# Optimization experiments

Hardware: AMD Instinct MI355X
Metric: run time of the kernel (lower is better)

## Reference

```python
import jax, jax.numpy as jnp
import numpy as np

R = 32
EPS = 0.0
BN_EPS = 1e-5


def _voxelize(features, idx):
    # features: [C, N], idx: [N] int32 flat voxel index in [0, R^3)
    V = R * R * R
    pts = features.T  # [N, C]
    sums = jax.ops.segment_sum(pts, idx, num_segments=V)          # [V, C]
    cnts = jax.ops.segment_sum(jnp.ones_like(idx, jnp.float32), idx, num_segments=V)  # [V]
    avg = sums / jnp.maximum(cnts, 1.0)[:, None]
    mx = jax.ops.segment_max(pts, idx, num_segments=V)            # [V, C], -inf for empty
    mx = jnp.where(cnts[:, None] > 0, mx, 0.0)
    return avg, mx, cnts


def reference(features, coords, conv_w, conv_b, bn_gamma, bn_beta, bn_mean, bn_var):
    B, C, N = features.shape
    # --- coordinate normalization (coords detached in original) ---
    nc = coords - jnp.mean(coords, axis=2, keepdims=True)          # [B,3,N]
    norms = jnp.linalg.norm(nc, axis=1, keepdims=True)             # [B,1,N]
    denom = jnp.max(norms, axis=2, keepdims=True) * 2.0 + EPS      # [B,1,1]
    nc = nc / denom + 0.5
    nc = jnp.clip(nc * R, 0.0, R - 1)                              # [B,3,N]
    vox = jnp.round(nc).astype(jnp.int32)                          # [B,3,N]
    idx = vox[:, 0] * (R * R) + vox[:, 1] * R + vox[:, 2]          # [B,N]
    # --- dual scatter reduction (avg + max) per batch ---
    avg, mx, _ = jax.vmap(_voxelize)(features, idx)                # [B, V, C] each
    fea = jnp.concatenate([mx, avg], axis=-1)                      # [B, V, 2C]
    # --- 1x1 Conv3d == channel matmul ---
    y = jnp.einsum('bvc,oc->bvo', fea, conv_w) + conv_b            # [B, V, C]
    # --- BatchNorm3d (eval mode) ---
    y = (y - bn_mean) * (bn_gamma / jnp.sqrt(bn_var + BN_EPS)) + bn_beta
    # --- Swish ---
    y = y * jax.nn.sigmoid(y)
    out = jnp.transpose(y, (0, 2, 1)).reshape(B, C, R, R, R)
    return out, nc


def setup_inputs() -> dict:
    key = jax.random.key(0)
    ks = jax.random.split(key, 8)
    B, C, N = 8, 240, 16384
    return {
        'features': jax.random.normal(ks[0], (B, C, N), jnp.float32),
        'coords': jax.random.normal(ks[1], (B, 3, N), jnp.float32),
        'conv_w': jax.random.normal(ks[2], (C, 2 * C), jnp.float32) * 0.05,
        'conv_b': jax.random.normal(ks[3], (C,), jnp.float32) * 0.05,
        'bn_gamma': jnp.ones((C,), jnp.float32),
        'bn_beta': jnp.zeros((C,), jnp.float32),
        'bn_mean': jnp.zeros((C,), jnp.float32),
        'bn_var': jax.random.uniform(ks[4], (C,), jnp.float32, 0.5, 1.5),
    }
```

## Files before the change

kernel.cpp:

```cpp
#include <hip/hip_runtime.h>
#include <math.h>

#define RR 32
#define V 32768
#define C 240
#define N 16384
#define B 8
#define K2C 480
#define GZ 16
#define NGRP 2048
#define FPAD 488
#define EBUF 512

typedef __attribute__((ext_vector_type(8))) short bf16x8;
typedef __attribute__((ext_vector_type(4))) float f32x4;

__device__ __forceinline__ unsigned short f2bf(float x) {
    unsigned u = __float_as_uint(x);
    u += 0x7fffu + ((u >> 16) & 1u);
    return (unsigned short)(u >> 16);
}

__global__ __launch_bounds__(256) void prep_kernel(const float* __restrict__ feat,
                                                   unsigned short* __restrict__ featT,
                                                   const float* __restrict__ coords,
                                                   float* __restrict__ stats,
                                                   int* __restrict__ hist,
                                                   int* __restrict__ wlcnt,
                                                   const float* __restrict__ w,
                                                   unsigned short* __restrict__ w_bf) {
    __shared__ float t[C][33];
    int blk = blockIdx.x;
    int tid = threadIdx.x;
    if (blk < 4096) {
        int bx = blk & 511, b = blk >> 9;
        int n0 = bx * 32;
        int l = tid;
        const float* fb = feat + (size_t)b * C * N;
        unsigned short* fTb = featT + (size_t)b * N * C;
        int nl = l & 31, cs = l >> 5;
#pragma unroll
        for (int p = 0; p < 30; ++p) {
            int c = p * 8 + cs;
            t[c][nl] = fb[(size_t)c * N + n0 + nl];
        }
        __syncthreads();
        int ci = l & 127;
        int nh = l >> 7;
#pragma unroll
        for (int p = 0; p < 16; ++p) {
            int n = 2 * p + nh;
            if (ci < 120) {
                unsigned lo = f2bf(t[2 * ci][n]);
                unsigned hi = f2bf(t[2 * ci + 1][n]);
                *(unsigned*)&fTb[(size_t)(n0 + n) * C + 2 * ci] = lo | (hi << 16);
            }
        }
        return;
    }
    if (blk < 4352) {
        int tt = (blk - 4096) * 256 + tid;
        int4 z4 = {0, 0, 0, 0};
        ((int4*)hist)[tt] = z4;
        if (tt < 57600) {
            unsigned lo = f2bf(w[2 * tt]);
            unsigned hi = f2bf(w[2 * tt + 1]);
            ((unsigned*)w_bf)[tt] = lo | (hi << 16);
        }
        if (tt < 2 * B) wlcnt[tt] = 0;
        return;
    }
    int b = blk - 4352;
    const float* cb = coords + (size_t)b * 3 * N;
    __shared__ float red[256];
    float m[3];
    for (int d = 0; d < 3; ++d) {
        float s = 0.f;
        for (int n = tid; n < N; n += 256) s += cb[d * N + n];
        red[tid] = s; __syncthreads();
        for (int w2 = 128; w2 > 0; w2 >>= 1) { if (tid < w2) red[tid] += red[tid + w2]; __syncthreads(); }
        m[d] = red[0] / (float)N;
        __syncthreads();
    }
    float mx = 0.f;
    for (int n = tid; n < N; n += 256) {
        float dx = cb[0 * N + n] - m[0];
        float dy = cb[1 * N + n] - m[1];
        float dz = cb[2 * N + n] - m[2];
        mx = fmaxf(mx, dx * dx + dy * dy + dz * dz);
    }
    red[tid] = mx; __syncthreads();
    for (int w2 = 128; w2 > 0; w2 >>= 1) { if (tid < w2) red[tid] = fmaxf(red[tid], red[tid + w2]); __syncthreads(); }
    if (tid == 0) {
        stats[b * 4 + 0] = m[0];
        stats[b * 4 + 1] = m[1];
        stats[b * 4 + 2] = m[2];
        stats[b * 4 + 3] = 2.f * sqrtf(red[0]);
    }
}

__global__ __launch_bounds__(256) void nc_idx_kernel(const float* __restrict__ coords,
                                                     const float* __restrict__ stats,
                                                     float* __restrict__ nc_out,
                                                     int* __restrict__ idxbuf,
                                                     int* __restrict__ hist) {
    int t = blockIdx.x * 256 + threadIdx.x;
    int b = t >> 14;
    int n = t & (N - 1);
    float denom = stats[b * 4 + 3];
    int v[3];
#pragma unroll
    for (int d = 0; d < 3; ++d) {
        float x = coords[((size_t)b * 3 + d) * N + n];
        float t0 = (x - stats[b * 4 + d]) / denom + 0.5f;
        t0 = t0 * (float)RR;
        t0 = fminf(fmaxf(t0, 0.f), (float)(RR - 1));
        nc_out[((size_t)b * 3 + d) * N + n] = t0;
        v[d] = (int)rintf(t0);
    }
    int iv = v[0] * (RR * RR) + v[1] * RR + v[2];
    idxbuf[t] = iv;
    atomicAdd(hist + b * V + iv, 1);
}

__global__ __launch_bounds__(1024) void prefix_kernel(const int* __restrict__ hist,
                                                      int* __restrict__ starts,
                                                      int* __restrict__ cursor,
                                                      int* __restrict__ wl,
                                                      int* __restrict__ wlcnt) {
    __shared__ int part[1024];
    int b = blockIdx.x, t = threadIdx.x;
    int base = b * V + t * 32;
    const int4* hp = (const int4*)(hist + base);
    int4 h[8];
#pragma unroll
    for (int j = 0; j < 8; ++j) h[j] = hp[j];
    int pcA = h[0].x + h[0].y + h[0].z + h[0].w + h[1].x + h[1].y + h[1].z + h[1].w
            + h[2].x + h[2].y + h[2].z + h[2].w + h[3].x + h[3].y + h[3].z + h[3].w;
    int pcB = h[4].x + h[4].y + h[4].z + h[4].w + h[5].x + h[5].y + h[5].z + h[5].w
            + h[6].x + h[6].y + h[6].z + h[6].w + h[7].x + h[7].y + h[7].z + h[7].w;
    int s = pcA + pcB;
    if (pcA > 0) { int p = atomicAdd(wlcnt + b, 1); wl[b * NGRP + p] = 2 * t; }
    if (pcB > 0) { int p = atomicAdd(wlcnt + b, 1); wl[b * NGRP + p] = 2 * t + 1; }
    if (pcA == 0 && pcB == 0) { int q = atomicAdd(wlcnt + B + b, 1); wl[b * NGRP + NGRP - 1 - q] = (2 * t) | 0x10000; }
    else if (pcA == 0)        { int q = atomicAdd(wlcnt + B + b, 1); wl[b * NGRP + NGRP - 1 - q] = 2 * t; }
    else if (pcB == 0)        { int q = atomicAdd(wlcnt + B + b, 1); wl[b * NGRP + NGRP - 1 - q] = 2 * t + 1; }
    part[t] = s; __syncthreads();
    for (int off = 1; off < 1024; off <<= 1) {
        int x = (t >= off) ? part[t - off] : 0;
        __syncthreads();
        part[t] += x;
        __syncthreads();
    }
    int run = part[t] - s;
    int4* sp = (int4*)(starts + base);
    int4* cp = (int4*)(cursor + base);
#pragma unroll
    for (int j = 0; j < 8; ++j) {
        int4 o;
        o.x = run; run += h[j].x;
        o.y = run; run += h[j].y;
        o.z = run; run += h[j].z;
        o.w = run; run += h[j].w;
        sp[j] = o; cp[j] = o;
    }
}

__global__ __launch_bounds__(256) void plist_kernel(const int* __restrict__ idxbuf,
                                                    int* __restrict__ cursor,
                                                    int* __restrict__ ptlist) {
    int t = blockIdx.x * 256 + threadIdx.x;
    int b = t >> 14;
    int n = t & (N - 1);
    int iv = idxbuf[t];
    int pos = atomicAdd(cursor + b * V + iv, 1);
    ptlist[(b << 14) + pos] = (n << 5) | (iv & 31);
}

#define PREFETCH(U, Z0, Z1, basei)                                          \
    {                                                                       \
        Z0 = 0u; Z1 = 0u;                                                   \
        _Pragma("unroll")                                                   \
        for (int j = 0; j < 16; ++j) {                                      \
            int idx = basei + j; idx = (idx < mm) ? idx : mm - 1;           \
            int e = ebuf[idx];                                              \
            U[j] = fT[(size_t)(e >> 5) * C + c];                            \
            unsigned zz = (unsigned)(e & 15);                               \
            if (j < 8) Z0 |= zz << (4 * j); else Z1 |= zz << (4 * (j - 8)); \
        }                                                                   \
    }

#define PROCESS(U, Z0, Z1, basei)                                           \
    {                                                                       \
        _Pragma("unroll")                                                   \
        for (int j = 0; j < 16; ++j) {                                      \
            if (basei + j < mm) {                                           \
                int zj = (int)(((j < 8 ? Z0 : Z1) >> (4 * (j & 7))) & 15u); \
                if (zj != curz) {                                           \
                    if (curz >= 0) {                                        \
                        fea_s[rb + curz][c] = f2bf(mx0);                    \
                        fea_s[rb + curz][C + c] = f2bf(s0 * rcp_s[rb + curz]); \
                    }                                                       \
                    curz = zj; s0 = 0.f; mx0 = -INFINITY;                   \
                }                                                           \
                float f = __uint_as_float(((unsigned)U[j]) << 16);          \
                s0 += f; mx0 = fmaxf(mx0, f);                               \
            }                                                               \
        }                                                                   \
    }

__global__ __launch_bounds__(256, 4) void column_kernel(
    const unsigned short* __restrict__ featT,
    const int* __restrict__ ptlist,
    const int* __restrict__ starts,
    const int* __restrict__ hist,
    const unsigned short* __restrict__ w_bf,
    const float* __restrict__ cbias, const float* __restrict__ gamma,
    const float* __restrict__ beta, const float* __restrict__ mean,
    const float* __restrict__ var,
    const int* __restrict__ wl, const int* __restrict__ wlcnt,
    float* __restrict__ out) {
    const int bx = blockIdx.x, b = blockIdx.y;
    const int nw = wlcnt[b];
    const int npair = (nw + 1) >> 1;
    const int ntot = npair + wlcnt[B + b];
    if (bx >= ntot) return;
    const bool isfill = (bx >= npair);
    const int tid = threadIdx.x;
    float* outb = out + (size_t)b * C * V;

    __shared__ float A_s[C], B_s[C], y0_s[C], rcp_s[2 * GZ];
    __shared__ unsigned short fea_s[2 * GZ][FPAD];
    __shared__ int cnt_s[2 * GZ];
    __shared__ int ebuf[EBUF];

    int wle0, wle1 = 0;
    bool has1 = false;
    if (isfill) {
        wle0 = wl[b * NGRP + NGRP - 1 - (bx - npair)];
    } else {
        wle0 = wl[b * NGRP + 2 * bx];
        has1 = (2 * bx + 1) < nw;
        wle1 = has1 ? wl[b * NGRP + 2 * bx + 1] : wle0;
    }
    const int v00 = (wle0 & 0xffff) * GZ;
    const int v01 = (wle1 & 0xffff) * GZ;

    if (tid < C) {
        float sc = gamma[tid] * rsqrtf(var[tid] + 1e-5f);
        A_s[tid] = sc;
        float b0 = (cbias[tid] - mean[tid]) * sc + beta[tid];
        B_s[tid] = b0;
        y0_s[tid] = b0 / (1.f + __expf(-b0));
    }
    if (!isfill && tid < 2 * GZ) {
        int c0;
        if (tid < GZ) c0 = hist[b * V + v00 + tid];
        else          c0 = has1 ? hist[b * V + v01 + (tid - GZ)] : 0;
        cnt_s[tid] = c0;
        rcp_s[tid] = 1.f / (float)max(c0, 1);
    }
    __syncthreads();

    if (isfill) {
        if (wle0 >> 16) {
            for (int i = tid; i < C * 8; i += 256) {
                int o = i >> 3, q = i & 7;
                float y = y0_s[o];
                float4 f4 = {y, y, y, y};
                *(float4*)&outb[(size_t)o * V + v00 + q * 4] = f4;
            }
        } else {
            for (int i = tid; i < C * 4; i += 256) {
                int o = i >> 2, q = i & 3;
                float y = y0_s[o];
                float4 f4 = {y, y, y, y};
                *(float4*)&outb[(size_t)o * V + v00 + q * 4] = f4;
            }
        }
        return;
    }

    int pc0 = 0, pc1 = 0;
#pragma unroll
    for (int z = 0; z < GZ; ++z) { pc0 += cnt_s[z]; pc1 += cnt_s[GZ + z]; }

    for (int i = tid; i < 2 * GZ * FPAD / 2; i += 256) ((unsigned*)fea_s)[i] = 0u;

    const int c = tid;
    const bool act = tid < C;
    const unsigned short* fT = featT + (size_t)b * N * C;

#pragma unroll 1
    for (int grp = 0; grp < 2; ++grp) {
        const int pc = grp ? pc1 : pc0;
        if (pc == 0) continue;
        const int rb = grp << 4;
        const int pos = starts[b * V + (grp ? v01 : v00)];
        const int* pl = ptlist + (b << 14) + pos;
        float s0 = 0.f, mx0 = -INFINITY;
        int curz = -1;
        for (int base = 0; base < pc; base += EBUF) {
            int mm = min(EBUF, pc - base);
            __syncthreads();
            for (int i = tid; i < mm; i += 256) ebuf[i] = pl[base + i];
            __syncthreads();
            if (act) {
                unsigned short uA[16], uB[16];
                unsigned zA0 = 0, zA1 = 0, zB0 = 0, zB1 = 0;
                PREFETCH(uA, zA0, zA1, 0);
                for (int i0 = 0; i0 < mm; i0 += 32) {
                    if (i0 + 16 < mm) PREFETCH(uB, zB0, zB1, i0 + 16);
                    PROCESS(uA, zA0, zA1, i0);
                    if (i0 + 32 < mm) PREFETCH(uA, zA0, zA1, i0 + 32);
                    PROCESS(uB, zB0, zB1, i0 + 16);
                }
            }
        }
        if (act && curz >= 0) {
            fea_s[rb + curz][c] = f2bf(mx0);
            fea_s[rb + curz][C + c] = f2bf(s0 * rcp_s[rb + curz]);
        }
    }
    __syncthreads();

    const int lane = tid & 63, wave = tid >> 6;
    const int mcnt = (wave == 3) ? 3 : 4;
    const int zl = lane & 15;
    const int koff = (lane >> 4) * 8;
    const int rbase = (lane >> 4) * 4;

    f32x4 acc0[4], acc1[4];
#pragma unroll
    for (int i = 0; i < 4; ++i) { acc0[i] = (f32x4){0.f, 0.f, 0.f, 0.f}; acc1[i] = (f32x4){0.f, 0.f, 0.f, 0.f}; }

#pragma unroll
    for (int kc = 0; kc < 15; ++kc) {
        const int kg = kc * 32 + koff;
        bf16x8 bfr0 = *(const bf16x8*)&fea_s[zl][kg];
        bf16x8 bfr1 = *(const bf16x8*)&fea_s[GZ + zl][kg];
        const unsigned short* wp = w_bf + (size_t)(wave * 64 + zl) * K2C + kg;
#pragma unroll
        for (int mt = 0; mt < 4; ++mt) {
            if (mt < mcnt) {
                bf16x8 afr = *(const bf16x8*)(wp + (size_t)mt * 16 * K2C);
                acc0[mt] = __builtin_amdgcn_mfma_f32_16x16x32_bf16(afr, bfr0, acc0[mt], 0, 0, 0);
                acc1[mt] = __builtin_amdgcn_mfma_f32_16x16x32_bf16(afr, bfr1, acc1[mt], 0, 0, 0);
            }
        }
    }

    const int vv0 = v00 + zl, vv1 = v01 + zl;
#pragma unroll
    for (int mt = 0; mt < 4; ++mt) {
        if (mt < mcnt) {
#pragma unroll
            for (int r = 0; r < 4; ++r) {
                int o = (wave * 4 + mt) * 16 + rbase + r;
                float y = acc0[mt][r] * A_s[o] + B_s[o];
                y = y / (1.f + __expf(-y));
                outb[(size_t)o * V + vv0] = y;
                if (has1) {
                    float y1 = acc1[mt][r] * A_s[o] + B_s[o];
                    y1 = y1 / (1.f + __expf(-y1));
                    outb[(size_t)o * V + vv1] = y1;
                }
            }
        }
    }
}

extern "C" void kernel_launch(void* const* d_in, const int* in_sizes, int n_in,
                              void* d_out, int out_size, void* d_ws, size_t ws_size,
                              hipStream_t stream) {
    const float* features = (const float*)d_in[0];
    const float* coords   = (const float*)d_in[1];
    const float* conv_w   = (const float*)d_in[2];
    const float* conv_b   = (const float*)d_in[3];
    const float* gamma    = (const float*)d_in[4];
    const float* beta     = (const float*)d_in[5];
    const float* mean     = (const float*)d_in[6];
    const float* var      = (const float*)d_in[7];

    float* out    = (float*)d_out;
    float* nc_out = out + (size_t)B * C * V;

    char* ws = (char*)d_ws;
    size_t off = 0;
    auto carve = [&](size_t bytes) { char* p = ws + off; off += (bytes + 255) & ~(size_t)255; return p; };
    int*            hist   = (int*)carve((size_t)B * V * 4);
    float*          stats  = (float*)carve(B * 4 * 4);
    int*            idxbuf = (int*)carve((size_t)B * N * 4);
    int*            starts = (int*)carve((size_t)B * V * 4);
    int*            cursor = (int*)carve((size_t)B * V * 4);
    int*            ptlist = (int*)carve((size_t)B * N * 4);
    int*            wl     = (int*)carve((size_t)B * NGRP * 4);
    int*            wlcnt  = (int*)carve((size_t)2 * B * 4);
    unsigned short* w_bf   = (unsigned short*)carve((size_t)C * K2C * 2);
    unsigned short* featT  = (unsigned short*)carve((size_t)B * N * C * 2);
    (void)off;

    prep_kernel<<<4360, 256, 0, stream>>>(features, featT, coords, stats, hist, wlcnt, conv_w, w_bf);
    nc_idx_kernel<<<(B * N) / 256, 256, 0, stream>>>(coords, stats, nc_out, idxbuf, hist);
    prefix_kernel<<<B, 1024, 0, stream>>>(hist, starts, cursor, wl, wlcnt);
    plist_kernel<<<(B * N) / 256, 256, 0, stream>>>(idxbuf, cursor, ptlist);
    column_kernel<<<dim3(NGRP, B), 256, 0, stream>>>(
        featT, ptlist, starts, hist, w_bf,
        conv_b, gamma, beta, mean, var, wl, wlcnt, out);
    (void)in_sizes; (void)n_in; (void)out_size;
}
```

Before: 565.4 us.

## Process both voxel groups concurrently with two channels per thread

The gather/reduce phase in the column kernel now splits the block into two halves, each half handling one of the two voxel groups at the same time, instead of looping over the groups one after the other. Each thread loads two adjacent bf16 channels as a single 32-bit load and keeps two sets of running sum and max, writing packed pairs into shared memory. The aim is to halve the serialized gather passes and increase bytes per load, at the cost of two ebuf staging buffers, more registers per thread, and idle lanes (channel pairs 120-127) in each half.

```diff
diff --git a/kernel.cpp b/kernel.cpp
--- a/kernel.cpp
+++ b/kernel.cpp
@@ -177,20 +177,20 @@
     ptlist[(b << 14) + pos] = (n << 5) | (iv & 31);
 }
 
-#define PREFETCH(U, Z0, Z1, basei)                                          \
+#define PF2(U, Z0, Z1, basei)                                               \
     {                                                                       \
         Z0 = 0u; Z1 = 0u;                                                   \
         _Pragma("unroll")                                                   \
         for (int j = 0; j < 16; ++j) {                                      \
             int idx = basei + j; idx = (idx < mm) ? idx : mm - 1;           \
-            int e = ebuf[idx];                                              \
-            U[j] = fT[(size_t)(e >> 5) * C + c];                            \
+            int e = ebg[idx];                                               \
+            U[j] = *(const unsigned*)&fT[(size_t)(e >> 5) * C + cc2];       \
             unsigned zz = (unsigned)(e & 15);                               \
             if (j < 8) Z0 |= zz << (4 * j); else Z1 |= zz << (4 * (j - 8)); \
         }                                                                   \
     }
 
-#define PROCESS(U, Z0, Z1, basei)                                           \
+#define PR2(U, Z0, Z1, basei)                                               \
     {                                                                       \
         _Pragma("unroll")                                                   \
         for (int j = 0; j < 16; ++j) {                                      \
@@ -198,13 +198,19 @@
                 int zj = (int)(((j < 8 ? Z0 : Z1) >> (4 * (j & 7))) & 15u); \
                 if (zj != curz) {                                           \
                     if (curz >= 0) {                                        \
-                        fea_s[rb + curz][c] = f2bf(mx0);                    \
-                        fea_s[rb + curz][C + c] = f2bf(s0 * rcp_s[rb + curz]); \
+                        float rc = rcp_s[rb + curz];                        \
+                        *(unsigned*)&fea_s[rb + curz][cc2] =                \
+                            (unsigned)f2bf(mx0) | ((unsigned)f2bf(mx1) << 16); \
+                        *(unsigned*)&fea_s[rb + curz][C + cc2] =            \
+                            (unsigned)f2bf(s0 * rc) | ((unsigned)f2bf(s1 * rc) << 16); \
                     }                                                       \
-                    curz = zj; s0 = 0.f; mx0 = -INFINITY;                   \
+                    curz = zj; s0 = s1 = 0.f; mx0 = mx1 = -INFINITY;        \
                 }                                                           \
-                float f = __uint_as_float(((unsigned)U[j]) << 16);          \
-                s0 += f; mx0 = fmaxf(mx0, f);                               \
+                unsigned u = U[j];                                          \
+                float flo = __uint_as_float(u << 16);                       \
+                float fhi = __uint_as_float(u & 0xffff0000u);               \
+                s0 += flo; s1 += fhi;                                       \
+                mx0 = fmaxf(mx0, flo); mx1 = fmaxf(mx1, fhi);               \
             }                                                               \
         }                                                                   \
     }
@@ -232,7 +238,7 @@
     __shared__ float A_s[C], B_s[C], y0_s[C], rcp_s[2 * GZ];
     __shared__ unsigned short fea_s[2 * GZ][FPAD];
     __shared__ int cnt_s[2 * GZ];
-    __shared__ int ebuf[EBUF];
+    __shared__ int ebuf0[EBUF], ebuf1[EBUF];
 
     int wle0, wle1 = 0;
     bool has1 = false;
@@ -287,44 +293,47 @@
 
     for (int i = tid; i < 2 * GZ * FPAD / 2; i += 256) ((unsigned*)fea_s)[i] = 0u;
 
-    const int c = tid;
-    const bool act = tid < C;
     const unsigned short* fT = featT + (size_t)b * N * C;
-
-#pragma unroll 1
-    for (int grp = 0; grp < 2; ++grp) {
-        const int pc = grp ? pc1 : pc0;
-        if (pc == 0) continue;
-        const int rb = grp << 4;
-        const int pos = starts[b * V + (grp ? v01 : v00)];
-        const int* pl = ptlist + (b << 14) + pos;
-        float s0 = 0.f, mx0 = -INFINITY;
-        int curz = -1;
-        for (int base = 0; base < pc; base += EBUF) {
-            int mm = min(EBUF, pc - base);
-            __syncthreads();
-            for (int i = tid; i < mm; i += 256) ebuf[i] = pl[base + i];
-            __syncthreads();
-            if (act) {
-                unsigned short uA[16], uB[16];
-                unsigned zA0 = 0, zA1 = 0, zB0 = 0, zB1 = 0;
-                PREFETCH(uA, zA0, zA1, 0);
-                for (int i0 = 0; i0 < mm; i0 += 32) {
-                    if (i0 + 16 < mm) PREFETCH(uB, zB0, zB1, i0 + 16);
-                    PROCESS(uA, zA0, zA1, i0);
-                    if (i0 + 32 < mm) PREFETCH(uA, zA0, zA1, i0 + 32);
-                    PROCESS(uB, zB0, zB1, i0 + 16);
-                }
-            }
-        }
-        if (act && curz >= 0) {
-            fea_s[rb + curz][c] = f2bf(mx0);
-            fea_s[rb + curz][C + c] = f2bf(s0 * rcp_s[rb + curz]);
-        }
+    const int lane = tid & 63, wave = tid >> 6;
+    const int grp = wave >> 1;
+    const int rb = grp << 4;
+    const int cc = tid & 127;
+    const int cc2 = cc << 1;
+    const bool act = cc < 120;
+    const int* pl0 = ptlist + (b << 14) + starts[b * V + v00];
+    const int* pl1 = ptlist + (b << 14) + starts[b * V + v01];
+    const int* ebg = grp ? ebuf1 : ebuf0;
+
+    float s0 = 0.f, s1 = 0.f, mx0 = -INFINITY, mx1 = -INFINITY;
+    int curz = -1;
+    const int pcmax = max(pc0, pc1);
+    for (int base = 0; base < pcmax; base += EBUF) {
+        int mm0 = min(EBUF, pc0 - base);
+        int mm1 = min(EBUF, pc1 - base);
+        __syncthreads();
+        for (int i = tid; i < mm0; i += 256) ebuf0[i] = pl0[base + i];
+        for (int i = tid; i < mm1; i += 256) ebuf1[i] = pl1[base + i];
+        __syncthreads();
+        int mm = grp ? mm1 : mm0;
+        if (act && mm > 0) {
+            unsigned uA[16], uB[16];
+            unsigned zA0 = 0, zA1 = 0, zB0 = 0, zB1 = 0;
+            PF2(uA, zA0, zA1, 0);
+            for (int i0 = 0; i0 < mm; i0 += 32) {
+                if (i0 + 16 < mm) PF2(uB, zB0, zB1, i0 + 16);
+                PR2(uA, zA0, zA1, i0);
+                if (i0 + 32 < mm) PF2(uA, zA0, zA1, i0 + 32);
+                PR2(uB, zB0, zB1, i0 + 16);
+            }
+        }
+    }
+    if (act && curz >= 0) {
+        float rc = rcp_s[rb + curz];
+        *(unsigned*)&fea_s[rb + curz][cc2] = (unsigned)f2bf(mx0) | ((unsigned)f2bf(mx1) << 16);
+        *(unsigned*)&fea_s[rb + curz][C + cc2] = (unsigned)f2bf(s0 * rc) | ((unsigned)f2bf(s1 * rc) << 16);
     }
     __syncthreads();
 
-    const int lane = tid & 63, wave = tid >> 6;
     const int mcnt = (wave == 3) ? 3 : 4;
     const int zl = lane & 15;
     const int koff = (lane >> 4) * 8;
```

Result: no change. 554.9 us (-1.9%).
